# Kernel tuning notes

Measured on AMD Instinct MI355X. Metric: run time of the kernel, lower is better.

Reference implementation:

```python
import jax, jax.numpy as jnp
import numpy as np

DIM = 1024
HEADS = 8
DIM_HEAD = 64
EPS = 1e-10
LN_EPS = 1e-5


def setup_inputs() -> dict:
    key = jax.random.key(0)
    k1, k2, k3 = jax.random.split(key, 3)
    b, n = 2, 4096
    x = jax.random.normal(k1, (b, n, DIM), dtype=jnp.float32)
    ln_gamma = jnp.ones((DIM,), dtype=jnp.float32)
    ln_beta = jnp.zeros((DIM,), dtype=jnp.float32)
    w_qkv = jax.random.normal(k2, (DIM, 3 * HEADS * DIM_HEAD), dtype=jnp.float32) * (DIM ** -0.5)
    w_out = jax.random.normal(k3, (HEADS * DIM_HEAD, DIM), dtype=jnp.float32) * ((HEADS * DIM_HEAD) ** -0.5)
    return {"x": x, "ln_gamma": ln_gamma, "ln_beta": ln_beta, "w_qkv": w_qkv, "w_out": w_out}


def _layernorm(x, gamma, beta):
    mu = jnp.mean(x, axis=-1, keepdims=True)
    var = jnp.var(x, axis=-1, keepdims=True)
    return (x - mu) * jax.lax.rsqrt(var + LN_EPS) * gamma + beta


def reference(x, ln_gamma, ln_beta, w_qkv, w_out):
    b, n, _ = x.shape
    h, dh = HEADS, DIM_HEAD
    scale = dh ** -0.5

    xn = _layernorm(x, ln_gamma, ln_beta)          # prenorm
    qkv = xn @ w_qkv                               # [b, n, 3*h*dh]
    q, k, v = jnp.split(qkv, 3, axis=-1)
    # [b, n, h*dh] -> [b, h, n, dh]
    def to_heads(t):
        return t.reshape(b, n, h, dh).transpose(0, 2, 1, 3)
    q, k, v = to_heads(q), to_heads(k), to_heads(v)

    # Ring/blockwise attention with online softmax is mathematically
    # equivalent to full softmax attention with an eps in the denominator.
    sim = jnp.einsum('bhid,bhjd->bhij', q, k) * scale   # [b, h, n, n]
    causal_mask = jnp.tril(jnp.ones((n, n), dtype=bool))
    sim = jnp.where(causal_mask, sim, -jnp.finfo(sim.dtype).max)

    m = jnp.max(sim, axis=-1, keepdims=True)            # row max (stable)
    p = jnp.exp(sim - m)
    denom = jnp.sum(p, axis=-1, keepdims=True) + EPS
    attn = p / denom

    out = jnp.einsum('bhij,bhjd->bhid', attn, v)        # [b, h, n, dh]
    out = out.transpose(0, 2, 1, 3).reshape(b, n, h * dh)
    return out @ w_out                                  # [b, n, dim]
```

## Files before the change

### kernel.cpp

```cpp
#include <hip/hip_runtime.h>
#include <hip/hip_bf16.h>
#include <stdint.h>

typedef unsigned short u16;
typedef unsigned int u32;

typedef __attribute__((ext_vector_type(8))) __bf16 bf16x8;
typedef __attribute__((ext_vector_type(4))) float f32x4;
typedef __attribute__((ext_vector_type(8))) u16 u16x8;

#define DIM 1024
#define SEQ 4096
#define NTOK 8192
#define NBH 16
#define NSLOT 96

static __device__ __forceinline__ float bf2f(u16 u) {
    union { u32 u; float f; } c; c.u = ((u32)u) << 16; return c.f;
}
static __device__ __forceinline__ u16 f2bf(float f) {
    union { float f; u32 u; } c; c.f = f;
    u32 u = c.u;
    return (u16)((u + 0x7FFF + ((u >> 16) & 1)) >> 16);
}
static __device__ __forceinline__ u16 cvt_bf16(float f) {
    union { __bf16 b; u16 u; } c; c.b = (__bf16)f;
    return c.u;
}
static __device__ __forceinline__ u32 pack_bf16(float lo, float hi) {
    return (u32)cvt_bf16(lo) | ((u32)cvt_bf16(hi) << 16);
}
static __device__ __forceinline__ f32x4 mfma_bf16(bf16x8 a, bf16x8 b, f32x4 c) {
    return __builtin_amdgcn_mfma_f32_16x16x32_bf16(a, b, c, 0, 0, 0);
}

typedef const __attribute__((address_space(1))) unsigned int* gptr_t;
typedef __attribute__((address_space(3))) unsigned int* lptr_t;

__global__ __launch_bounds__(256) void ln_kernel(const float* __restrict__ x,
                                                 const float* __restrict__ g,
                                                 const float* __restrict__ bta,
                                                 u16* __restrict__ xn) {
    int row = blockIdx.x;
    int tid = threadIdx.x;
    float4 v = ((const float4*)(x + (size_t)row * DIM))[tid];
    float f[4] = {v.x, v.y, v.z, v.w};
    float s = 0.f, s2 = 0.f;
#pragma unroll
    for (int i = 0; i < 4; i++) { s += f[i]; s2 += f[i] * f[i]; }
#pragma unroll
    for (int m = 1; m < 64; m <<= 1) { s += __shfl_xor(s, m); s2 += __shfl_xor(s2, m); }
    __shared__ float red[8];
    int w = tid >> 6;
    if ((tid & 63) == 0) { red[w * 2] = s; red[w * 2 + 1] = s2; }
    __syncthreads();
    s  = red[0] + red[2] + red[4] + red[6];
    s2 = red[1] + red[3] + red[5] + red[7];
    float mu = s * (1.f / DIM);
    float var = s2 * (1.f / DIM) - mu * mu;
    float rstd = rsqrtf(var + 1e-5f);
    u16 o[4];
#pragma unroll
    for (int i = 0; i < 4; i++) {
        int c = tid * 4 + i;
        o[i] = f2bf((f[i] - mu) * rstd * g[c] + bta[c]);
    }
    *(uint64_t*)(xn + (size_t)row * DIM + tid * 4) = *(uint64_t*)o;
}

__global__ __launch_bounds__(256) void transpose_kernel(const float* __restrict__ src,
                                                        u16* __restrict__ dst,
                                                        int R, int C) {
    __shared__ float t[32][33];
    int lx = threadIdx.x & 31, ly = threadIdx.x >> 5;
    int c = blockIdx.x * 32 + lx;
#pragma unroll
    for (int i = 0; i < 32; i += 8)
        t[ly + i][lx] = src[(size_t)(blockIdx.y * 32 + ly + i) * C + c];
    __syncthreads();
    int rr = blockIdx.y * 32 + lx;
#pragma unroll
    for (int i = 0; i < 32; i += 8)
        dst[(size_t)(blockIdx.x * 32 + ly + i) * R + rr] = f2bf(t[lx][ly + i]);
}

template <int K>
static __device__ __forceinline__ void gemm_core(const u16* __restrict__ A,
                                                 const u16* __restrict__ B,
                                                 int rowBase, int colBase,
                                                 u16* A_lds, u16* B_lds,
                                                 f32x4 acc[4][4]) {
    int tid = threadIdx.x;
    int lane = tid & 63;
    int l15 = lane & 15, q4 = lane >> 4;
    int w = tid >> 6;
    int wm = w >> 1, wn = w & 1;
#pragma unroll
    for (int mt = 0; mt < 4; mt++)
#pragma unroll
        for (int nt = 0; nt < 4; nt++) acc[mt][nt] = (f32x4){0.f, 0.f, 0.f, 0.f};

    char* Ab = (char*)A_lds;
    char* Bb = (char*)B_lds;

    for (int k0 = 0; k0 < K; k0 += 32) {
        __syncthreads();
#pragma unroll
        for (int i = 0; i < 2; i++) {
            int c = i * 256 + tid;
            int r = c >> 2;
            int piece = (c & 3) * 8;
            const u16* gA = A + (size_t)(rowBase + r) * K + k0 + piece;
            const u16* gB = B + (size_t)(colBase + r) * K + k0 + piece;
            unsigned ldsOff = (unsigned)(i * 4096 + w * 1024);
            __builtin_amdgcn_global_load_lds((gptr_t)gA, (lptr_t)(Ab + ldsOff), 16, 0, 0);
            __builtin_amdgcn_global_load_lds((gptr_t)gB, (lptr_t)(Bb + ldsOff), 16, 0, 0);
        }
        __syncthreads();
        bf16x8 a[4], b[4];
#pragma unroll
        for (int mt = 0; mt < 4; mt++)
            a[mt] = *(const bf16x8*)(A_lds + (wm * 64 + mt * 16 + l15) * 32 + q4 * 8);
#pragma unroll
        for (int nt = 0; nt < 4; nt++)
            b[nt] = *(const bf16x8*)(B_lds + (wn * 64 + nt * 16 + l15) * 32 + q4 * 8);
#pragma unroll
        for (int mt = 0; mt < 4; mt++)
#pragma unroll
            for (int nt = 0; nt < 4; nt++)
                acc[mt][nt] = mfma_bf16(a[mt], b[nt], acc[mt][nt]);
    }
}

__global__ __launch_bounds__(256) void gemm_qkv_kernel(const u16* __restrict__ xn,
                                                       const u16* __restrict__ wT,
                                                       u16* __restrict__ qb,
                                                       u16* __restrict__ kb,
                                                       u16* __restrict__ vbT) {
    __shared__ u16 A_lds[128 * 32];
    __shared__ u16 B_lds[128 * 32];
    f32x4 acc[4][4];
    gemm_core<1024>(xn, wT, blockIdx.x * 128, blockIdx.y * 128, A_lds, B_lds, acc);
    int lane = threadIdx.x & 63;
    int w = threadIdx.x >> 6;
    int wm = w >> 1, wn = w & 1;
    const float SC = 0.125f * 1.44269504f;
#pragma unroll
    for (int mt = 0; mt < 4; mt++) {
#pragma unroll
        for (int nt = 0; nt < 4; nt++) {
#pragma unroll
            for (int r = 0; r < 4; r++) {
                int m = blockIdx.x * 128 + wm * 64 + mt * 16 + (lane >> 4) * 4 + r;
                int n = blockIdx.y * 128 + wn * 64 + nt * 16 + (lane & 15);
                int piece = n >> 9;
                int c = n & 511;
                int h = c >> 6;
                int d = c & 63;
                int bi = m >> 12;
                int nn = m & 4095;
                int bh = bi * 8 + h;
                float av = acc[mt][nt][r];
                if (piece == 0)      qb[((size_t)(bh * SEQ + nn) << 6) + d] = f2bf(av * SC);
                else if (piece == 1) kb[((size_t)(bh * SEQ + nn) << 6) + d] = f2bf(av);
                else                 vbT[((size_t)(bh * 64 + d) << 12) + nn] = f2bf(av);
            }
        }
    }
}

__global__ __launch_bounds__(256) void gemm_out_kernel(const u16* __restrict__ aout,
                                                       const u16* __restrict__ wT,
                                                       float* __restrict__ out) {
    __shared__ u16 A_lds[128 * 32];
    __shared__ u16 B_lds[128 * 32];
    f32x4 acc[4][4];
    gemm_core<512>(aout, wT, blockIdx.x * 128, blockIdx.y * 128, A_lds, B_lds, acc);
    int lane = threadIdx.x & 63;
    int w = threadIdx.x >> 6;
    int wm = w >> 1, wn = w & 1;
#pragma unroll
    for (int mt = 0; mt < 4; mt++) {
#pragma unroll
        for (int nt = 0; nt < 4; nt++) {
#pragma unroll
            for (int r = 0; r < 4; r++) {
                int m = blockIdx.x * 128 + wm * 64 + mt * 16 + (lane >> 4) * 4 + r;
                int n = blockIdx.y * 128 + wn * 64 + nt * 16 + (lane & 15);
                out[(size_t)m * DIM + n] = acc[mt][nt][r];
            }
        }
    }
}

#define ASTR 72
#define PSTR 72

__global__ __launch_bounds__(256, 4) void attn_partial_kernel(const u16* __restrict__ qb,
                                                              const u16* __restrict__ kb,
                                                              const u16* __restrict__ vbT,
                                                              u16* __restrict__ part,
                                                              float* __restrict__ lpart) {
    __shared__ u16 K_lds[64 * ASTR];
    __shared__ u16 VT_lds[64 * ASTR];
    __shared__ u16 P_lds[4 * 16 * PSTR];

    int bid = blockIdx.x;
    int bs = (bid & 7) * 192 + (bid >> 3);
    int idx = NBH * NSLOT - 1 - bs;
    int bh = idx / NSLOT;
    int s  = idx - bh * NSLOT;
    int qt, ci;
    if (s < 32) { qt = s; ci = 0; }
    else        { int t = s - 32; qt = 32 + (t >> 1); ci = t & 1; }
    int kt0 = ci * 32;
    int kt1 = min(kt0 + 31, qt);

    int tid = threadIdx.x;
    int lane = tid & 63;
    int l15 = lane & 15, g = lane >> 4;
    int w = tid >> 6;

    const u16* Kp0 = kb + (size_t)bh * SEQ * 64;
    const u16* VTp = vbT + ((size_t)bh * 64) * SEQ;

    const u16* Qp = qb + ((size_t)bh * SEQ + qt * 64 + w * 16 + l15) * 64;
    bf16x8 bQ0 = *(const bf16x8*)(Qp + g * 8);
    bf16x8 bQ1 = *(const bf16x8*)(Qp + 32 + g * 8);

    f32x4 Oacc[4];
    f32x4 l_acc = (f32x4){0.f, 0.f, 0.f, 0.f};
#pragma unroll
    for (int vt = 0; vt < 4; vt++) Oacc[vt] = (f32x4){0.f, 0.f, 0.f, 0.f};

    const __bf16 one_bf = (__bf16)1.0f;
    bf16x8 vones = {one_bf, one_bf, one_bf, one_bf, one_bf, one_bf, one_bf, one_bf};

    u16* Pw = P_lds + w * 16 * PSTR;

    int c0 = tid, c1 = tid + 256;
    int r0 = c0 >> 3, kc0 = (c0 & 7) * 8;
    int r1 = c1 >> 3, kc1 = (c1 & 7) * 8;

    u16x8 krA0, krA1, vrA0, vrA1;
    {
        const u16* Kp = Kp0 + (size_t)kt0 * 64 * 64;
        krA0 = *(const u16x8*)(Kp + r0 * 64 + kc0);
        krA1 = *(const u16x8*)(Kp + r1 * 64 + kc1);
        vrA0 = *(const u16x8*)(VTp + (size_t)r0 * SEQ + kt0 * 64 + kc0);
        vrA1 = *(const u16x8*)(VTp + (size_t)r1 * SEQ + kt0 * 64 + kc1);
    }

    for (int kt = kt0; kt <= kt1; kt++) {
        __syncthreads();
        *(u16x8*)(K_lds + r0 * ASTR + kc0) = krA0;
        *(u16x8*)(K_lds + r1 * ASTR + kc1) = krA1;
        *(u16x8*)(VT_lds + r0 * ASTR + kc0) = vrA0;
        *(u16x8*)(VT_lds + r1 * ASTR + kc1) = vrA1;
        int ktn = (kt < kt1) ? kt + 1 : kt1;
        const u16* Kpn = Kp0 + (size_t)ktn * 64 * 64;
        u16x8 krB0 = *(const u16x8*)(Kpn + r0 * 64 + kc0);
        u16x8 krB1 = *(const u16x8*)(Kpn + r1 * 64 + kc1);
        u16x8 vrB0 = *(const u16x8*)(VTp + (size_t)r0 * SEQ + ktn * 64 + kc0);
        u16x8 vrB1 = *(const u16x8*)(VTp + (size_t)r1 * SEQ + ktn * 64 + kc1);
        __syncthreads();

        f32x4 sv[4];
#pragma unroll
        for (int mt = 0; mt < 4; mt++) {
            bf16x8 a0 = *(const bf16x8*)(K_lds + (mt * 16 + l15) * ASTR + g * 8);
            bf16x8 a1 = *(const bf16x8*)(K_lds + (mt * 16 + l15) * ASTR + 32 + g * 8);
            f32x4 z = (f32x4){0.f, 0.f, 0.f, 0.f};
            z = mfma_bf16(a0, bQ0, z);
            z = mfma_bf16(a1, bQ1, z);
            sv[mt] = z;
        }

        if (kt != qt) {
#pragma unroll
            for (int mt = 0; mt < 4; mt++) {
                float p0 = __builtin_amdgcn_exp2f(sv[mt][0]);
                float p1 = __builtin_amdgcn_exp2f(sv[mt][1]);
                float p2 = __builtin_amdgcn_exp2f(sv[mt][2]);
                float p3 = __builtin_amdgcn_exp2f(sv[mt][3]);
                uint2 t;
                t.x = pack_bf16(p0, p1);
                t.y = pack_bf16(p2, p3);
                *(uint2*)(Pw + l15 * PSTR + mt * 16 + g * 4) = t;
            }
        } else {
            int qg = w * 16 + l15;
#pragma unroll
            for (int mt = 0; mt < 4; mt++) {
                float p[4];
#pragma unroll
                for (int r = 0; r < 4; r++) {
                    int kg = mt * 16 + g * 4 + r;
                    p[r] = (kg <= qg) ? __builtin_amdgcn_exp2f(sv[mt][r]) : 0.f;
                }
                uint2 t;
                t.x = pack_bf16(p[0], p[1]);
                t.y = pack_bf16(p[2], p[3]);
                *(uint2*)(Pw + l15 * PSTR + mt * 16 + g * 4) = t;
            }
        }

        bf16x8 aP0 = *(const bf16x8*)(Pw + l15 * PSTR + g * 8);
        bf16x8 aP1 = *(const bf16x8*)(Pw + l15 * PSTR + 32 + g * 8);
        l_acc = mfma_bf16(aP0, vones, l_acc);
        l_acc = mfma_bf16(aP1, vones, l_acc);
#pragma unroll
        for (int vt = 0; vt < 4; vt++) {
            bf16x8 bV0 = *(const bf16x8*)(VT_lds + (vt * 16 + l15) * ASTR + g * 8);
            bf16x8 bV1 = *(const bf16x8*)(VT_lds + (vt * 16 + l15) * ASTR + 32 + g * 8);
            Oacc[vt] = mfma_bf16(aP0, bV0, Oacc[vt]);
            Oacc[vt] = mfma_bf16(aP1, bV1, Oacc[vt]);
        }

        krA0 = krB0; krA1 = krB1; vrA0 = vrB0; vrA1 = vrB1;
    }

    u16* po = part + (size_t)idx * 4096;
#pragma unroll
    for (int vt = 0; vt < 4; vt++)
#pragma unroll
        for (int r = 0; r < 4; r++) {
            int q = w * 16 + g * 4 + r;
            int d = vt * 16 + l15;
            po[q * 64 + d] = f2bf(Oacc[vt][r]);
        }
    if (l15 == 0) {
#pragma unroll
        for (int r = 0; r < 4; r++)
            lpart[(size_t)idx * 64 + w * 16 + g * 4 + r] = l_acc[r];
    }
}

__global__ __launch_bounds__(256) void attn_combine_kernel(const u16* __restrict__ part,
                                                           const float* __restrict__ lpart,
                                                           u16* __restrict__ aout) {
    int bid = blockIdx.x;
    int bh = bid >> 6;
    int qt = bid & 63;
    int nc = 1 + (qt >> 5);
    int sb = bh * NSLOT + (qt < 32 ? qt : 32 + (qt - 32) * 2);

    int t = threadIdx.x;
    int q = t >> 2;
    int dg = (t & 3) * 16;

    float acc[16];
#pragma unroll
    for (int j = 0; j < 16; j++) acc[j] = 0.f;
    float ll = 0.f;
    for (int ci = 0; ci < nc; ci++) {
        const u16* pp = part + (size_t)(sb + ci) * 4096 + q * 64 + dg;
        u16x8 v0 = *(const u16x8*)pp;
        u16x8 v1 = *(const u16x8*)(pp + 8);
#pragma unroll
        for (int j = 0; j < 8; j++) { acc[j] += bf2f(v0[j]); acc[8 + j] += bf2f(v1[j]); }
        ll += lpart[(size_t)(sb + ci) * 64 + q];
    }
    float inv = 1.f / (ll + 1e-10f);
    int b = bh >> 3, h = bh & 7;
    size_t row = (size_t)(b * SEQ + qt * 64 + q);
    u16 o[16];
#pragma unroll
    for (int j = 0; j < 16; j++) o[j] = f2bf(acc[j] * inv);
    u16* dst = aout + row * 512 + h * 64 + dg;
    *(u16x8*)dst = *(u16x8*)o;
    *(u16x8*)(dst + 8) = *(u16x8*)(o + 8);
}

extern "C" void kernel_launch(void* const* d_in, const int* in_sizes, int n_in,
                              void* d_out, int out_size, void* d_ws, size_t ws_size,
                              hipStream_t stream) {
    const float* x    = (const float*)d_in[0];
    const float* g    = (const float*)d_in[1];
    const float* bta  = (const float*)d_in[2];
    const float* wqkv = (const float*)d_in[3];
    const float* wout = (const float*)d_in[4];
    float* out = (float*)d_out;

    char* ws = (char*)d_ws;
    size_t off = 0;
    auto alloc = [&](size_t bytes) {
        void* p = ws + off;
        off += (bytes + 255) & ~(size_t)255;
        return p;
    };
    u16* xn    = (u16*)alloc((size_t)NTOK * DIM * 2);
    u16* wqkvT = (u16*)alloc((size_t)1536 * 1024 * 2);
    u16* woutT = (u16*)alloc((size_t)1024 * 512 * 2);
    u16* qb    = (u16*)alloc((size_t)NBH * SEQ * 64 * 2);
    u16* kb    = (u16*)alloc((size_t)NBH * SEQ * 64 * 2);
    u16* vbT   = (u16*)alloc((size_t)NBH * SEQ * 64 * 2);
    u16* part  = xn;
    float* lpart = (float*)(xn + (size_t)NBH * NSLOT * 4096);
    u16* aout  = qb;

    ln_kernel<<<NTOK, 256, 0, stream>>>(x, g, bta, xn);
    transpose_kernel<<<dim3(1536 / 32, 1024 / 32), 256, 0, stream>>>(wqkv, wqkvT, 1024, 1536);
    transpose_kernel<<<dim3(1024 / 32, 512 / 32), 256, 0, stream>>>(wout, woutT, 512, 1024);
    gemm_qkv_kernel<<<dim3(64, 12), 256, 0, stream>>>(xn, wqkvT, qb, kb, vbT);
    attn_partial_kernel<<<NBH * NSLOT, 256, 0, stream>>>(qb, kb, vbT, part, lpart);
    attn_combine_kernel<<<NBH * 64, 256, 0, stream>>>(part, lpart, aout);
    gemm_out_kernel<<<dim3(64, 8), 256, 0, stream>>>(aout, woutT, out);
}
```

Before: 230.6 us.

## Run attention partial with one wave per block using async LDS double buffering

The attention partial kernel goes from four waves per 64-row query tile to a single wave that owns all 64 query rows. K and V tiles are loaded straight into LDS with global_load_lds into a double buffer, using XOR-swizzled layouts instead of padding. Since only one wave touches the LDS, the __syncthreads barriers are replaced by vmcnt waits. The aim is to remove barrier and register-staging cost and overlap the next tile's load with compute. The trade-off is a quarter as many waves per block, far more accumulator registers per wave, and reliance on a hard-coded vmcnt count that must match the number of issued loads.

```diff
diff --git a/kernel.cpp b/kernel.cpp
--- a/kernel.cpp
+++ b/kernel.cpp
@@ -193,17 +193,15 @@
     }
 }
 
-#define ASTR 72
-#define PSTR 72
-
-__global__ __launch_bounds__(256, 4) void attn_partial_kernel(const u16* __restrict__ qb,
-                                                              const u16* __restrict__ kb,
-                                                              const u16* __restrict__ vbT,
-                                                              u16* __restrict__ part,
-                                                              float* __restrict__ lpart) {
-    __shared__ u16 K_lds[64 * ASTR];
-    __shared__ u16 VT_lds[64 * ASTR];
-    __shared__ u16 P_lds[4 * 16 * PSTR];
+
+__global__ __launch_bounds__(64) void attn_partial_kernel(const u16* __restrict__ qb,
+                                                          const u16* __restrict__ kb,
+                                                          const u16* __restrict__ vbT,
+                                                          u16* __restrict__ part,
+                                                          float* __restrict__ lpart) {
+    __shared__ u16 K_lds[2][4096];
+    __shared__ u16 V_lds[2][4096];
+    __shared__ u16 P_lds[4096];
 
     int bid = blockIdx.x;
     int bs = (bid & 7) * 192 + (bid >> 3);
@@ -216,123 +214,162 @@
     int kt0 = ci * 32;
     int kt1 = min(kt0 + 31, qt);
 
-    int tid = threadIdx.x;
-    int lane = tid & 63;
-    int l15 = lane & 15, g = lane >> 4;
-    int w = tid >> 6;
+    int l = threadIdx.x;
+    int l15 = l & 15, g = l >> 4;
+    int swz = (l15 & 7) << 3;
 
     const u16* Kp0 = kb + (size_t)bh * SEQ * 64;
-    const u16* VTp = vbT + ((size_t)bh * 64) * SEQ;
-
-    const u16* Qp = qb + ((size_t)bh * SEQ + qt * 64 + w * 16 + l15) * 64;
-    bf16x8 bQ0 = *(const bf16x8*)(Qp + g * 8);
-    bf16x8 bQ1 = *(const bf16x8*)(Qp + 32 + g * 8);
-
-    f32x4 Oacc[4];
-    f32x4 l_acc = (f32x4){0.f, 0.f, 0.f, 0.f};
-#pragma unroll
-    for (int vt = 0; vt < 4; vt++) Oacc[vt] = (f32x4){0.f, 0.f, 0.f, 0.f};
+    const u16* VTp = vbT + (size_t)bh * 64 * SEQ;
+    const u16* Qp  = qb + ((size_t)bh * SEQ + (size_t)qt * 64) * 64;
+
+    bf16x8 bQ[4][2];
+#pragma unroll
+    for (int qs = 0; qs < 4; qs++) {
+        const u16* qp = Qp + (qs * 16 + l15) * 64 + g * 8;
+        bQ[qs][0] = *(const bf16x8*)qp;
+        bQ[qs][1] = *(const bf16x8*)(qp + 32);
+    }
+
+    int srow = l >> 3;
+    int scol = ((l & 7) ^ srow) * 8;
+
+    {
+        const u16* Kt = Kp0 + (size_t)kt0 * 4096;
+#pragma unroll
+        for (int i = 0; i < 8; i++) {
+            __builtin_amdgcn_global_load_lds((gptr_t)(Kt + (i * 8 + srow) * 64 + scol),
+                                             (lptr_t)((char*)&K_lds[0][0] + i * 1024), 16, 0, 0);
+            __builtin_amdgcn_global_load_lds((gptr_t)(VTp + (size_t)(i * 8 + srow) * SEQ + kt0 * 64 + scol),
+                                             (lptr_t)((char*)&V_lds[0][0] + i * 1024), 16, 0, 0);
+        }
+    }
+
+    f32x4 Oacc[4][4];
+    f32x4 l_acc[4];
+#pragma unroll
+    for (int qs = 0; qs < 4; qs++) {
+        l_acc[qs] = (f32x4){0.f, 0.f, 0.f, 0.f};
+#pragma unroll
+        for (int vt = 0; vt < 4; vt++) Oacc[qs][vt] = (f32x4){0.f, 0.f, 0.f, 0.f};
+    }
 
     const __bf16 one_bf = (__bf16)1.0f;
     bf16x8 vones = {one_bf, one_bf, one_bf, one_bf, one_bf, one_bf, one_bf, one_bf};
 
-    u16* Pw = P_lds + w * 16 * PSTR;
-
-    int c0 = tid, c1 = tid + 256;
-    int r0 = c0 >> 3, kc0 = (c0 & 7) * 8;
-    int r1 = c1 >> 3, kc1 = (c1 & 7) * 8;
-
-    u16x8 krA0, krA1, vrA0, vrA1;
-    {
-        const u16* Kp = Kp0 + (size_t)kt0 * 64 * 64;
-        krA0 = *(const u16x8*)(Kp + r0 * 64 + kc0);
-        krA1 = *(const u16x8*)(Kp + r1 * 64 + kc1);
-        vrA0 = *(const u16x8*)(VTp + (size_t)r0 * SEQ + kt0 * 64 + kc0);
-        vrA1 = *(const u16x8*)(VTp + (size_t)r1 * SEQ + kt0 * 64 + kc1);
-    }
-
+    int rd0 = (g * 8) ^ swz;
+    int rd1 = (32 + g * 8) ^ swz;
+
+    int cur = 0;
     for (int kt = kt0; kt <= kt1; kt++) {
-        __syncthreads();
-        *(u16x8*)(K_lds + r0 * ASTR + kc0) = krA0;
-        *(u16x8*)(K_lds + r1 * ASTR + kc1) = krA1;
-        *(u16x8*)(VT_lds + r0 * ASTR + kc0) = vrA0;
-        *(u16x8*)(VT_lds + r1 * ASTR + kc1) = vrA1;
-        int ktn = (kt < kt1) ? kt + 1 : kt1;
-        const u16* Kpn = Kp0 + (size_t)ktn * 64 * 64;
-        u16x8 krB0 = *(const u16x8*)(Kpn + r0 * 64 + kc0);
-        u16x8 krB1 = *(const u16x8*)(Kpn + r1 * 64 + kc1);
-        u16x8 vrB0 = *(const u16x8*)(VTp + (size_t)r0 * SEQ + ktn * 64 + kc0);
-        u16x8 vrB1 = *(const u16x8*)(VTp + (size_t)r1 * SEQ + ktn * 64 + kc1);
-        __syncthreads();
-
-        f32x4 sv[4];
+        if (kt < kt1) {
+            const u16* Kt = Kp0 + (size_t)(kt + 1) * 4096;
+            char* kd = (char*)&K_lds[cur ^ 1][0];
+            char* vd = (char*)&V_lds[cur ^ 1][0];
+#pragma unroll
+            for (int i = 0; i < 8; i++) {
+                __builtin_amdgcn_global_load_lds((gptr_t)(Kt + (i * 8 + srow) * 64 + scol),
+                                                 (lptr_t)(kd + i * 1024), 16, 0, 0);
+                __builtin_amdgcn_global_load_lds((gptr_t)(VTp + (size_t)(i * 8 + srow) * SEQ + (kt + 1) * 64 + scol),
+                                                 (lptr_t)(vd + i * 1024), 16, 0, 0);
+            }
+            asm volatile("s_waitcnt vmcnt(16)" ::: "memory");
+        } else {
+            asm volatile("s_waitcnt vmcnt(0)" ::: "memory");
+        }
+        __builtin_amdgcn_sched_barrier(0);
+
+        const u16* KL = &K_lds[cur][0];
+        const u16* VL = &V_lds[cur][0];
+
+        bf16x8 ka[4][2];
 #pragma unroll
         for (int mt = 0; mt < 4; mt++) {
-            bf16x8 a0 = *(const bf16x8*)(K_lds + (mt * 16 + l15) * ASTR + g * 8);
-            bf16x8 a1 = *(const bf16x8*)(K_lds + (mt * 16 + l15) * ASTR + 32 + g * 8);
-            f32x4 z = (f32x4){0.f, 0.f, 0.f, 0.f};
-            z = mfma_bf16(a0, bQ0, z);
-            z = mfma_bf16(a1, bQ1, z);
-            sv[mt] = z;
-        }
-
-        if (kt != qt) {
+            int row = mt * 16 + l15;
+            ka[mt][0] = *(const bf16x8*)(KL + row * 64 + rd0);
+            ka[mt][1] = *(const bf16x8*)(KL + row * 64 + rd1);
+        }
+
+#pragma unroll
+        for (int qs = 0; qs < 4; qs++) {
+            f32x4 sv[4];
 #pragma unroll
             for (int mt = 0; mt < 4; mt++) {
-                float p0 = __builtin_amdgcn_exp2f(sv[mt][0]);
-                float p1 = __builtin_amdgcn_exp2f(sv[mt][1]);
-                float p2 = __builtin_amdgcn_exp2f(sv[mt][2]);
-                float p3 = __builtin_amdgcn_exp2f(sv[mt][3]);
-                uint2 t;
-                t.x = pack_bf16(p0, p1);
-                t.y = pack_bf16(p2, p3);
-                *(uint2*)(Pw + l15 * PSTR + mt * 16 + g * 4) = t;
-            }
-        } else {
-            int qg = w * 16 + l15;
-#pragma unroll
-            for (int mt = 0; mt < 4; mt++) {
-                float p[4];
-#pragma unroll
-                for (int r = 0; r < 4; r++) {
-                    int kg = mt * 16 + g * 4 + r;
-                    p[r] = (kg <= qg) ? __builtin_amdgcn_exp2f(sv[mt][r]) : 0.f;
+                f32x4 z = (f32x4){0.f, 0.f, 0.f, 0.f};
+                z = mfma_bf16(ka[mt][0], bQ[qs][0], z);
+                z = mfma_bf16(ka[mt][1], bQ[qs][1], z);
+                sv[mt] = z;
+            }
+            int prow = qs * 16 + l15;
+            u16* pb = P_lds + prow * 64;
+            if (kt != qt) {
+#pragma unroll
+                for (int mt = 0; mt < 4; mt++) {
+                    uint2 t;
+                    t.x = pack_bf16(__builtin_amdgcn_exp2f(sv[mt][0]),
+                                    __builtin_amdgcn_exp2f(sv[mt][1]));
+                    t.y = pack_bf16(__builtin_amdgcn_exp2f(sv[mt][2]),
+                                    __builtin_amdgcn_exp2f(sv[mt][3]));
+                    *(uint2*)(pb + ((mt * 16 + g * 4) ^ swz)) = t;
                 }
-                uint2 t;
-                t.x = pack_bf16(p[0], p[1]);
-                t.y = pack_bf16(p[2], p[3]);
-                *(uint2*)(Pw + l15 * PSTR + mt * 16 + g * 4) = t;
-            }
-        }
-
-        bf16x8 aP0 = *(const bf16x8*)(Pw + l15 * PSTR + g * 8);
-        bf16x8 aP1 = *(const bf16x8*)(Pw + l15 * PSTR + 32 + g * 8);
-        l_acc = mfma_bf16(aP0, vones, l_acc);
-        l_acc = mfma_bf16(aP1, vones, l_acc);
+            } else {
+                int qg = qs * 16 + l15;
+#pragma unroll
+                for (int mt = 0; mt < 4; mt++) {
+                    float p[4];
+#pragma unroll
+                    for (int r = 0; r < 4; r++) {
+                        int kg = mt * 16 + g * 4 + r;
+                        p[r] = (kg <= qg) ? __builtin_amdgcn_exp2f(sv[mt][r]) : 0.f;
+                    }
+                    uint2 t;
+                    t.x = pack_bf16(p[0], p[1]);
+                    t.y = pack_bf16(p[2], p[3]);
+                    *(uint2*)(pb + ((mt * 16 + g * 4) ^ swz)) = t;
+                }
+            }
+        }
+
+        bf16x8 aP[4][2];
+#pragma unroll
+        for (int qs = 0; qs < 4; qs++) {
+            int prow = qs * 16 + l15;
+            aP[qs][0] = *(const bf16x8*)(P_lds + prow * 64 + rd0);
+            aP[qs][1] = *(const bf16x8*)(P_lds + prow * 64 + rd1);
+            l_acc[qs] = mfma_bf16(aP[qs][0], vones, l_acc[qs]);
+            l_acc[qs] = mfma_bf16(aP[qs][1], vones, l_acc[qs]);
+        }
+
 #pragma unroll
         for (int vt = 0; vt < 4; vt++) {
-            bf16x8 bV0 = *(const bf16x8*)(VT_lds + (vt * 16 + l15) * ASTR + g * 8);
-            bf16x8 bV1 = *(const bf16x8*)(VT_lds + (vt * 16 + l15) * ASTR + 32 + g * 8);
-            Oacc[vt] = mfma_bf16(aP0, bV0, Oacc[vt]);
-            Oacc[vt] = mfma_bf16(aP1, bV1, Oacc[vt]);
-        }
-
-        krA0 = krB0; krA1 = krB1; vrA0 = vrB0; vrA1 = vrB1;
+            int vrow = vt * 16 + l15;
+            bf16x8 bV0 = *(const bf16x8*)(VL + vrow * 64 + rd0);
+            bf16x8 bV1 = *(const bf16x8*)(VL + vrow * 64 + rd1);
+#pragma unroll
+            for (int qs = 0; qs < 4; qs++) {
+                Oacc[qs][vt] = mfma_bf16(aP[qs][0], bV0, Oacc[qs][vt]);
+                Oacc[qs][vt] = mfma_bf16(aP[qs][1], bV1, Oacc[qs][vt]);
+            }
+        }
+
+        cur ^= 1;
     }
 
     u16* po = part + (size_t)idx * 4096;
 #pragma unroll
-    for (int vt = 0; vt < 4; vt++)
-#pragma unroll
-        for (int r = 0; r < 4; r++) {
-            int q = w * 16 + g * 4 + r;
-            int d = vt * 16 + l15;
-            po[q * 64 + d] = f2bf(Oacc[vt][r]);
-        }
-    if (l15 == 0) {
-#pragma unroll
-        for (int r = 0; r < 4; r++)
-            lpart[(size_t)idx * 64 + w * 16 + g * 4 + r] = l_acc[r];
+    for (int qs = 0; qs < 4; qs++) {
+#pragma unroll
+        for (int vt = 0; vt < 4; vt++)
+#pragma unroll
+            for (int r = 0; r < 4; r++) {
+                int q = qs * 16 + g * 4 + r;
+                int d = vt * 16 + l15;
+                po[q * 64 + d] = f2bf(Oacc[qs][vt][r]);
+            }
+        if (l15 == 0) {
+#pragma unroll
+            for (int r = 0; r < 4; r++)
+                lpart[(size_t)idx * 64 + qs * 16 + g * 4 + r] = l_acc[qs][r];
+        }
     }
 }
 
@@ -403,7 +440,7 @@
     transpose_kernel<<<dim3(1536 / 32, 1024 / 32), 256, 0, stream>>>(wqkv, wqkvT, 1024, 1536);
     transpose_kernel<<<dim3(1024 / 32, 512 / 32), 256, 0, stream>>>(wout, woutT, 512, 1024);
     gemm_qkv_kernel<<<dim3(64, 12), 256, 0, stream>>>(xn, wqkvT, qb, kb, vbT);
-    attn_partial_kernel<<<NBH * NSLOT, 256, 0, stream>>>(qb, kb, vbT, part, lpart);
+    attn_partial_kernel<<<NBH * NSLOT, 64, 0, stream>>>(qb, kb, vbT, part, lpart);
     attn_combine_kernel<<<NBH * 64, 256, 0, stream>>>(part, lpart, aout);
     gemm_out_kernel<<<dim3(64, 8), 256, 0, stream>>>(aout, woutT, out);
 }
```

Measured after the change: 276.8 us. +20.1%, slower.

## Rebalance attention split-K into finer chunks and swizzle LDS tiles

Applied to the files above, without the earlier changes.

Splits each query tile's causal key range into up to four roughly equal chunks of at most 20 key tiles, replacing the old scheme of at most two chunks of 32. This raises the slot count from 96 to 136 per head and updates the combine kernel to match. It also replaces the padded LDS layouts for K, V and P with XOR-swizzled unpadded ones, and moves the next-tile global prefetch after the second barrier. The goal is shorter critical-path blocks for better load balance plus fewer LDS bank conflicts, at the cost of more partial outputs to write and combine, and it drops the occupancy hint from launch bounds.

```diff
diff --git a/kernel.cpp b/kernel.cpp
--- a/kernel.cpp
+++ b/kernel.cpp
@@ -13,7 +13,7 @@
 #define SEQ 4096
 #define NTOK 8192
 #define NBH 16
-#define NSLOT 96
+#define NSLOT 136
 
 static __device__ __forceinline__ float bf2f(u16 u) {
     union { u32 u; float f; } c; c.u = ((u32)u) << 16; return c.f;
@@ -193,40 +193,62 @@
     }
 }
 
-#define ASTR 72
-#define PSTR 72
-
-__global__ __launch_bounds__(256, 4) void attn_partial_kernel(const u16* __restrict__ qb,
-                                                              const u16* __restrict__ kb,
-                                                              const u16* __restrict__ vbT,
-                                                              u16* __restrict__ part,
-                                                              float* __restrict__ lpart) {
-    __shared__ u16 K_lds[64 * ASTR];
-    __shared__ u16 VT_lds[64 * ASTR];
-    __shared__ u16 P_lds[4 * 16 * PSTR];
+
+__global__ __launch_bounds__(256) void attn_partial_kernel(const u16* __restrict__ qb,
+                                                           const u16* __restrict__ kb,
+                                                           const u16* __restrict__ vbT,
+                                                           u16* __restrict__ part,
+                                                           float* __restrict__ lpart) {
+    __shared__ u16 K_lds[4096];
+    __shared__ u16 V_lds[4096];
+    __shared__ u16 P_lds[4][1024];
 
     int bid = blockIdx.x;
-    int bs = (bid & 7) * 192 + (bid >> 3);
+    int bs = (bid & 7) * 272 + (bid >> 3);
     int idx = NBH * NSLOT - 1 - bs;
     int bh = idx / NSLOT;
     int s  = idx - bh * NSLOT;
     int qt, ci;
-    if (s < 32) { qt = s; ci = 0; }
-    else        { int t = s - 32; qt = 32 + (t >> 1); ci = t & 1; }
-    int kt0 = ci * 32;
-    int kt1 = min(kt0 + 31, qt);
+    if (s < 20)       { qt = s; ci = 0; }
+    else if (s < 60)  { int t = s - 20;  qt = 20 + (t >> 1); ci = t & 1; }
+    else if (s < 120) { int t = s - 60;  qt = 40 + t / 3;    ci = t - (t / 3) * 3; }
+    else              { int t = s - 120; qt = 60 + (t >> 2); ci = t & 3; }
+    int nq = qt + 1;
+    int nc = (nq + 19) / 20;
+    int L  = nq / nc;
+    int R  = nq - L * nc;
+    int kt0 = ci * L + (ci < R ? ci : R);
+    int kt1 = kt0 + L + (ci < R ? 1 : 0) - 1;
 
     int tid = threadIdx.x;
     int lane = tid & 63;
     int l15 = lane & 15, g = lane >> 4;
     int w = tid >> 6;
+    int swz = (l15 & 7) << 3;
+    int rd0 = (g * 8) ^ swz;
+    int rd1 = (32 + g * 8) ^ swz;
 
     const u16* Kp0 = kb + (size_t)bh * SEQ * 64;
-    const u16* VTp = vbT + ((size_t)bh * 64) * SEQ;
-
-    const u16* Qp = qb + ((size_t)bh * SEQ + qt * 64 + w * 16 + l15) * 64;
-    bf16x8 bQ0 = *(const bf16x8*)(Qp + g * 8);
-    bf16x8 bQ1 = *(const bf16x8*)(Qp + 32 + g * 8);
+    const u16* VTp = vbT + (size_t)bh * 64 * SEQ;
+
+    const u16* qp = qb + ((size_t)bh * SEQ + (size_t)qt * 64 + w * 16 + l15) * 64;
+    bf16x8 bQ0 = *(const bf16x8*)(qp + g * 8);
+    bf16x8 bQ1 = *(const bf16x8*)(qp + 32 + g * 8);
+
+    int c0 = tid, c1 = tid + 256;
+    int r0 = c0 >> 3, g0 = c0 & 7;
+    int r1 = c1 >> 3, g1 = c1 & 7;
+    int wc0 = r0 * 64 + ((g0 ^ (r0 & 7)) * 8);
+    int wc1 = r1 * 64 + ((g1 ^ (r1 & 7)) * 8);
+
+    u16x8 krA0, krA1, vrA0, vrA1;
+    {
+        const u16* Kt = Kp0 + (size_t)kt0 * 4096;
+        krA0 = *(const u16x8*)(Kt + r0 * 64 + g0 * 8);
+        krA1 = *(const u16x8*)(Kt + r1 * 64 + g1 * 8);
+        vrA0 = *(const u16x8*)(VTp + (size_t)r0 * SEQ + kt0 * 64 + g0 * 8);
+        vrA1 = *(const u16x8*)(VTp + (size_t)r1 * SEQ + kt0 * 64 + g1 * 8);
+    }
 
     f32x4 Oacc[4];
     f32x4 l_acc = (f32x4){0.f, 0.f, 0.f, 0.f};
@@ -236,88 +258,75 @@
     const __bf16 one_bf = (__bf16)1.0f;
     bf16x8 vones = {one_bf, one_bf, one_bf, one_bf, one_bf, one_bf, one_bf, one_bf};
 
-    u16* Pw = P_lds + w * 16 * PSTR;
-
-    int c0 = tid, c1 = tid + 256;
-    int r0 = c0 >> 3, kc0 = (c0 & 7) * 8;
-    int r1 = c1 >> 3, kc1 = (c1 & 7) * 8;
-
-    u16x8 krA0, krA1, vrA0, vrA1;
-    {
-        const u16* Kp = Kp0 + (size_t)kt0 * 64 * 64;
-        krA0 = *(const u16x8*)(Kp + r0 * 64 + kc0);
-        krA1 = *(const u16x8*)(Kp + r1 * 64 + kc1);
-        vrA0 = *(const u16x8*)(VTp + (size_t)r0 * SEQ + kt0 * 64 + kc0);
-        vrA1 = *(const u16x8*)(VTp + (size_t)r1 * SEQ + kt0 * 64 + kc1);
-    }
+    u16* Pw = &P_lds[w][0];
 
     for (int kt = kt0; kt <= kt1; kt++) {
         __syncthreads();
-        *(u16x8*)(K_lds + r0 * ASTR + kc0) = krA0;
-        *(u16x8*)(K_lds + r1 * ASTR + kc1) = krA1;
-        *(u16x8*)(VT_lds + r0 * ASTR + kc0) = vrA0;
-        *(u16x8*)(VT_lds + r1 * ASTR + kc1) = vrA1;
+        *(u16x8*)(K_lds + wc0) = krA0;
+        *(u16x8*)(K_lds + wc1) = krA1;
+        *(u16x8*)(V_lds + wc0) = vrA0;
+        *(u16x8*)(V_lds + wc1) = vrA1;
+        __syncthreads();
         int ktn = (kt < kt1) ? kt + 1 : kt1;
-        const u16* Kpn = Kp0 + (size_t)ktn * 64 * 64;
-        u16x8 krB0 = *(const u16x8*)(Kpn + r0 * 64 + kc0);
-        u16x8 krB1 = *(const u16x8*)(Kpn + r1 * 64 + kc1);
-        u16x8 vrB0 = *(const u16x8*)(VTp + (size_t)r0 * SEQ + ktn * 64 + kc0);
-        u16x8 vrB1 = *(const u16x8*)(VTp + (size_t)r1 * SEQ + ktn * 64 + kc1);
-        __syncthreads();
+        {
+            const u16* Ktn = Kp0 + (size_t)ktn * 4096;
+            krA0 = *(const u16x8*)(Ktn + r0 * 64 + g0 * 8);
+            krA1 = *(const u16x8*)(Ktn + r1 * 64 + g1 * 8);
+            vrA0 = *(const u16x8*)(VTp + (size_t)r0 * SEQ + ktn * 64 + g0 * 8);
+            vrA1 = *(const u16x8*)(VTp + (size_t)r1 * SEQ + ktn * 64 + g1 * 8);
+        }
 
         f32x4 sv[4];
 #pragma unroll
-        for (int mt = 0; mt < 4; mt++) {
-            bf16x8 a0 = *(const bf16x8*)(K_lds + (mt * 16 + l15) * ASTR + g * 8);
-            bf16x8 a1 = *(const bf16x8*)(K_lds + (mt * 16 + l15) * ASTR + 32 + g * 8);
+        for (int nt = 0; nt < 4; nt++) {
+            int row = nt * 16 + l15;
+            bf16x8 a0 = *(const bf16x8*)(K_lds + row * 64 + rd0);
+            bf16x8 a1 = *(const bf16x8*)(K_lds + row * 64 + rd1);
             f32x4 z = (f32x4){0.f, 0.f, 0.f, 0.f};
             z = mfma_bf16(a0, bQ0, z);
             z = mfma_bf16(a1, bQ1, z);
-            sv[mt] = z;
+            sv[nt] = z;
         }
 
         if (kt != qt) {
 #pragma unroll
-            for (int mt = 0; mt < 4; mt++) {
-                float p0 = __builtin_amdgcn_exp2f(sv[mt][0]);
-                float p1 = __builtin_amdgcn_exp2f(sv[mt][1]);
-                float p2 = __builtin_amdgcn_exp2f(sv[mt][2]);
-                float p3 = __builtin_amdgcn_exp2f(sv[mt][3]);
+            for (int nt = 0; nt < 4; nt++) {
                 uint2 t;
-                t.x = pack_bf16(p0, p1);
-                t.y = pack_bf16(p2, p3);
-                *(uint2*)(Pw + l15 * PSTR + mt * 16 + g * 4) = t;
+                t.x = pack_bf16(__builtin_amdgcn_exp2f(sv[nt][0]),
+                                __builtin_amdgcn_exp2f(sv[nt][1]));
+                t.y = pack_bf16(__builtin_amdgcn_exp2f(sv[nt][2]),
+                                __builtin_amdgcn_exp2f(sv[nt][3]));
+                *(uint2*)(Pw + l15 * 64 + ((nt * 16 + g * 4) ^ swz)) = t;
             }
         } else {
             int qg = w * 16 + l15;
 #pragma unroll
-            for (int mt = 0; mt < 4; mt++) {
+            for (int nt = 0; nt < 4; nt++) {
                 float p[4];
 #pragma unroll
                 for (int r = 0; r < 4; r++) {
-                    int kg = mt * 16 + g * 4 + r;
-                    p[r] = (kg <= qg) ? __builtin_amdgcn_exp2f(sv[mt][r]) : 0.f;
+                    int kg = nt * 16 + g * 4 + r;
+                    p[r] = (kg <= qg) ? __builtin_amdgcn_exp2f(sv[nt][r]) : 0.f;
                 }
                 uint2 t;
                 t.x = pack_bf16(p[0], p[1]);
                 t.y = pack_bf16(p[2], p[3]);
-                *(uint2*)(Pw + l15 * PSTR + mt * 16 + g * 4) = t;
+                *(uint2*)(Pw + l15 * 64 + ((nt * 16 + g * 4) ^ swz)) = t;
             }
         }
 
-        bf16x8 aP0 = *(const bf16x8*)(Pw + l15 * PSTR + g * 8);
-        bf16x8 aP1 = *(const bf16x8*)(Pw + l15 * PSTR + 32 + g * 8);
+        bf16x8 aP0 = *(const bf16x8*)(Pw + l15 * 64 + rd0);
+        bf16x8 aP1 = *(const bf16x8*)(Pw + l15 * 64 + rd1);
         l_acc = mfma_bf16(aP0, vones, l_acc);
         l_acc = mfma_bf16(aP1, vones, l_acc);
 #pragma unroll
         for (int vt = 0; vt < 4; vt++) {
-            bf16x8 bV0 = *(const bf16x8*)(VT_lds + (vt * 16 + l15) * ASTR + g * 8);
-            bf16x8 bV1 = *(const bf16x8*)(VT_lds + (vt * 16 + l15) * ASTR + 32 + g * 8);
+            int vrow = vt * 16 + l15;
+            bf16x8 bV0 = *(const bf16x8*)(V_lds + vrow * 64 + rd0);
+            bf16x8 bV1 = *(const bf16x8*)(V_lds + vrow * 64 + rd1);
             Oacc[vt] = mfma_bf16(aP0, bV0, Oacc[vt]);
             Oacc[vt] = mfma_bf16(aP1, bV1, Oacc[vt]);
         }
-
-        krA0 = krB0; krA1 = krB1; vrA0 = vrB0; vrA1 = vrB1;
     }
 
     u16* po = part + (size_t)idx * 4096;
@@ -342,8 +351,12 @@
     int bid = blockIdx.x;
     int bh = bid >> 6;
     int qt = bid & 63;
-    int nc = 1 + (qt >> 5);
-    int sb = bh * NSLOT + (qt < 32 ? qt : 32 + (qt - 32) * 2);
+    int nc, base;
+    if (qt < 20)      { nc = 1; base = qt; }
+    else if (qt < 40) { nc = 2; base = 20 + (qt - 20) * 2; }
+    else if (qt < 60) { nc = 3; base = 60 + (qt - 40) * 3; }
+    else              { nc = 4; base = 120 + (qt - 60) * 4; }
+    int sb = bh * NSLOT + base;
 
     int t = threadIdx.x;
     int q = t >> 2;
```

Measured after the change: 216.1 us. -6.3%, faster.
